# Kernel tuning notes

Hardware: AMD Instinct MI355X
Metric: run time of the kernel (lower is better)

## Reference

```python
import jax, jax.numpy as jnp
import numpy as np

B, V, D = 8, 1024, 512
H = 8
HD = D // H
MAX_HOP = 8


def setup_inputs() -> dict:
    key = jax.random.key(0)
    ks = jax.random.split(key, 5)
    x = jax.random.normal(ks[0], (B, V, D), dtype=jnp.float32)
    w_qkv = jax.random.normal(ks[1], (D, 3 * D), dtype=jnp.float32) * (D ** -0.5)
    w_out = jax.random.normal(ks[2], (D, D), dtype=jnp.float32) * (D ** -0.5)
    b_out = jnp.zeros((D,), dtype=jnp.float32)
    rpe_bias = jax.random.normal(ks[3], (H, MAX_HOP + 1), dtype=jnp.float32) * 0.02
    hop_matrix = jax.random.randint(ks[4], (V, V), 0, MAX_HOP + 1, dtype=jnp.int32)
    return {"x": x, "w_qkv": w_qkv, "w_out": w_out, "b_out": b_out,
            "rpe_bias": rpe_bias, "hop_matrix": hop_matrix}


def reference(x, w_qkv, w_out, b_out, rpe_bias, hop_matrix):
    b, v, d = x.shape
    scale = HD ** -0.5
    qkv = x @ w_qkv                                   # [B, V, 3D]
    q, k, val = jnp.split(qkv, 3, axis=-1)
    # [B, V, D] -> [B, H, V, HD]
    def split_heads(t):
        return t.reshape(b, v, H, HD).transpose(0, 2, 1, 3)
    q, k, val = split_heads(q), split_heads(k), split_heads(val)
    scores = jnp.einsum('bhvd,bhwd->bhvw', q, k)      # [B, H, V, V]
    bias = rpe_bias[:, hop_matrix]                    # gather -> [H, V, V]
    attn = jax.nn.softmax((scores + bias[None]) * scale, axis=-1)
    out_heads = jnp.einsum('bhvw,bhwd->bhvd', attn, val)
    out = out_heads.transpose(0, 2, 1, 3).reshape(b, v, d)
    out = out @ w_out + b_out
    return out, attn
```

## Files before the change

### kernel.cpp

```cpp
#include <hip/hip_runtime.h>

typedef __attribute__((ext_vector_type(8))) short bf16x8;
typedef __attribute__((ext_vector_type(4))) float f32x4;

#define MFMA16(A,B,C) __builtin_amdgcn_mfma_f32_16x16x32_bf16(A,B,C,0,0,0)

__device__ __forceinline__ unsigned short f2bf(float f){
  unsigned int u = __float_as_uint(f);
  u += 0x7FFFu + ((u >> 16) & 1u);
  return (unsigned short)(u >> 16);
}
__device__ __forceinline__ float bf2f(unsigned short s){
  return __uint_as_float(((unsigned int)s) << 16);
}
__device__ __forceinline__ int swz(int row, int kbyte){
  return (row * 128 + kbyte) ^ ((row & 7) << 4);
}

__global__ __launch_bounds__(256) void k_prep(
    const float* __restrict__ w_qkv, const float* __restrict__ w_out,
    unsigned short* __restrict__ wqT, unsigned short* __restrict__ woT)
{
  int idx = blockIdx.x * 256 + threadIdx.x;
  if (idx < 1536 * 512) {
    int n = idx >> 9, kq = idx & 511;
    wqT[idx] = f2bf(w_qkv[(size_t)kq * 1536 + n]);
  } else {
    int j = idx - 1536 * 512;
    int n = j >> 9, kq = j & 511;
    woT[j] = f2bf(w_out[(size_t)kq * 512 + n]);
  }
}

__global__ __launch_bounds__(256) void k_qkv(
    const float* __restrict__ x, const unsigned short* __restrict__ wqT,
    unsigned short* __restrict__ q, unsigned short* __restrict__ k_,
    unsigned short* __restrict__ valT)
{
  __shared__ char lds[32768];
  char* At = lds; char* Bt = lds + 16384;
  const int tid = threadIdx.x;
  const int wid = tid >> 6, lane = tid & 63, g = lane >> 4, r = lane & 15;
  const int wm = wid >> 1, wn = wid & 1;
  const int m0 = blockIdx.x * 128, n0 = blockIdx.y * 128;

  f32x4 acc[4][4];
#pragma unroll
  for (int a = 0; a < 4; ++a)
#pragma unroll
    for (int b = 0; b < 4; ++b) acc[a][b] = (f32x4){0.f, 0.f, 0.f, 0.f};

  for (int kt = 0; kt < 8; ++kt) {
    const int k0 = kt * 64;
    __syncthreads();
#pragma unroll
    for (int it = 0; it < 8; ++it) {
      int c = tid + it * 256;
      int row = c >> 4, c4 = c & 15;
      float4 xv = *reinterpret_cast<const float4*>(x + (size_t)(m0 + row) * 512 + k0 + c4 * 4);
      uint2 hv;
      hv.x = (unsigned)f2bf(xv.x) | ((unsigned)f2bf(xv.y) << 16);
      hv.y = (unsigned)f2bf(xv.z) | ((unsigned)f2bf(xv.w) << 16);
      *reinterpret_cast<uint2*>(At + swz(row, c4 * 8)) = hv;
    }
#pragma unroll
    for (int it = 0; it < 4; ++it) {
      int c = tid + it * 256;
      int row = c >> 3, c8 = c & 7;
      *reinterpret_cast<uint4*>(Bt + swz(row, c8 * 16)) =
          *reinterpret_cast<const uint4*>(wqT + (size_t)(n0 + row) * 512 + k0 + c8 * 8);
    }
    __syncthreads();
#pragma unroll
    for (int kk = 0; kk < 2; ++kk) {
      bf16x8 af[4], bf[4];
      const int kb = (kk * 32 + 8 * g) * 2;
#pragma unroll
      for (int mi = 0; mi < 4; ++mi)
        af[mi] = *reinterpret_cast<const bf16x8*>(At + swz(wm * 64 + mi * 16 + r, kb));
#pragma unroll
      for (int ni = 0; ni < 4; ++ni)
        bf[ni] = *reinterpret_cast<const bf16x8*>(Bt + swz(wn * 64 + ni * 16 + r, kb));
#pragma unroll
      for (int mi = 0; mi < 4; ++mi)
#pragma unroll
        for (int ni = 0; ni < 4; ++ni)
          acc[mi][ni] = MFMA16(af[mi], bf[ni], acc[mi][ni]);
    }
  }
  const int s = n0 >> 9;
#pragma unroll
  for (int mi = 0; mi < 4; ++mi)
#pragma unroll
    for (int ni = 0; ni < 4; ++ni)
#pragma unroll
      for (int i = 0; i < 4; ++i) {
        int m = m0 + wm * 64 + mi * 16 + 4 * g + i;
        int n = n0 + wn * 64 + ni * 16 + r;
        int b = m >> 10, v = m & 1023;
        int cc = n & 511, h = cc >> 6, d = cc & 63;
        int bh = b * 8 + h;
        unsigned short bfv = f2bf(acc[mi][ni][i]);
        if (s == 2)      valT[((size_t)bh * 64 + d) * 1024 + v] = bfv;
        else if (s == 0) q [((size_t)bh * 1024 + v) * 64 + d] = bfv;
        else             k_[((size_t)bh * 1024 + v) * 64 + d] = bfv;
      }
}

__global__ __launch_bounds__(256) void k_attn(
    const unsigned short* __restrict__ q, const unsigned short* __restrict__ k_,
    const unsigned short* __restrict__ valT,
    const float* __restrict__ rpe_bias, const int* __restrict__ hop,
    float* __restrict__ attn, unsigned short* __restrict__ oh)
{
  __shared__ float S[16 * 1028];
  __shared__ float rpe[9];
  const int tid = threadIdx.x;
  const int wid = tid >> 6, lane = tid & 63, g = lane >> 4, r = lane & 15;
  const int blk = blockIdx.x;
  const int vt = blk & 63, bh = blk >> 6, h = bh & 7;
  const int v0 = vt * 16;
  if (tid < 9) rpe[tid] = rpe_bias[h * 9 + tid];

  const unsigned short* qp = q + ((size_t)bh * 1024 + v0) * 64;
  bf16x8 qf[2];
#pragma unroll
  for (int kk = 0; kk < 2; ++kk)
    qf[kk] = *reinterpret_cast<const bf16x8*>(qp + r * 64 + kk * 32 + 8 * g);
  __syncthreads();

  const unsigned short* kb = k_ + (size_t)bh * 65536;
  for (int ct = 0; ct < 16; ++ct) {
    int cb = wid * 256 + ct * 16;
    f32x4 acc = (f32x4){0.f, 0.f, 0.f, 0.f};
#pragma unroll
    for (int kk = 0; kk < 2; ++kk) {
      bf16x8 kf = *reinterpret_cast<const bf16x8*>(kb + (size_t)(cb + r) * 64 + kk * 32 + 8 * g);
      acc = MFMA16(qf[kk], kf, acc);
    }
    int wcol = cb + r;
#pragma unroll
    for (int i = 0; i < 4; ++i) {
      int vl = 4 * g + i;
      int hv = hop[(size_t)(v0 + vl) * 1024 + wcol];
      S[vl * 1028 + wcol] = (acc[i] + rpe[hv]) * 0.125f;
    }
  }
  __syncthreads();

#pragma unroll
  for (int rr = 0; rr < 4; ++rr) {
    int row = wid * 4 + rr;
    float* Sr = S + row * 1028;
    float e[16];
    float m = -1e30f;
#pragma unroll
    for (int j = 0; j < 16; ++j) { e[j] = Sr[lane + 64 * j]; m = fmaxf(m, e[j]); }
#pragma unroll
    for (int o = 32; o; o >>= 1) m = fmaxf(m, __shfl_xor(m, o, 64));
    float sum = 0.f;
#pragma unroll
    for (int j = 0; j < 16; ++j) { e[j] = __expf(e[j] - m); sum += e[j]; }
#pragma unroll
    for (int o = 32; o; o >>= 1) sum += __shfl_xor(sum, o, 64);
    float inv = 1.0f / sum;
    float* ar = attn + ((size_t)bh * 1024 + v0 + row) * 1024;
#pragma unroll
    for (int j = 0; j < 16; ++j) {
      float a = e[j] * inv;
      int col = lane + 64 * j;
      Sr[col] = a;
      ar[col] = a;
    }
  }
  __syncthreads();

  const unsigned short* vT = valT + ((size_t)bh * 64 + wid * 16) * 1024;
  f32x4 acc = (f32x4){0.f, 0.f, 0.f, 0.f};
  for (int kc = 0; kc < 32; ++kc) {
    const float* ap = S + r * 1028 + kc * 32 + 8 * g;
    float4 p0 = *reinterpret_cast<const float4*>(ap);
    float4 p1 = *reinterpret_cast<const float4*>(ap + 4);
    bf16x8 af;
    af[0] = (short)f2bf(p0.x); af[1] = (short)f2bf(p0.y);
    af[2] = (short)f2bf(p0.z); af[3] = (short)f2bf(p0.w);
    af[4] = (short)f2bf(p1.x); af[5] = (short)f2bf(p1.y);
    af[6] = (short)f2bf(p1.z); af[7] = (short)f2bf(p1.w);
    bf16x8 bfr = *reinterpret_cast<const bf16x8*>(vT + (size_t)r * 1024 + kc * 32 + 8 * g);
    acc = MFMA16(af, bfr, acc);
  }
  const int b = bh >> 3;
#pragma unroll
  for (int i = 0; i < 4; ++i) {
    size_t oi = ((size_t)(b * 1024 + v0 + 4 * g + i)) * 512 + h * 64 + wid * 16 + r;
    oh[oi] = f2bf(acc[i]);
  }
}

__global__ __launch_bounds__(256) void k_out(
    const unsigned short* __restrict__ oh, const unsigned short* __restrict__ woT,
    const float* __restrict__ b_out, float* __restrict__ out)
{
  __shared__ char lds[32768];
  char* At = lds; char* Bt = lds + 16384;
  const int tid = threadIdx.x;
  const int wid = tid >> 6, lane = tid & 63, g = lane >> 4, r = lane & 15;
  const int wm = wid >> 1, wn = wid & 1;
  const int m0 = blockIdx.x * 128, n0 = blockIdx.y * 128;

  f32x4 acc[4][4];
#pragma unroll
  for (int a = 0; a < 4; ++a)
#pragma unroll
    for (int b = 0; b < 4; ++b) acc[a][b] = (f32x4){0.f, 0.f, 0.f, 0.f};

  for (int kt = 0; kt < 8; ++kt) {
    const int k0 = kt * 64;
    __syncthreads();
#pragma unroll
    for (int it = 0; it < 4; ++it) {
      int c = tid + it * 256;
      int row = c >> 3, c8 = c & 7;
      *reinterpret_cast<uint4*>(At + swz(row, c8 * 16)) =
          *reinterpret_cast<const uint4*>(oh + (size_t)(m0 + row) * 512 + k0 + c8 * 8);
      *reinterpret_cast<uint4*>(Bt + swz(row, c8 * 16)) =
          *reinterpret_cast<const uint4*>(woT + (size_t)(n0 + row) * 512 + k0 + c8 * 8);
    }
    __syncthreads();
#pragma unroll
    for (int kk = 0; kk < 2; ++kk) {
      bf16x8 a4[4], b4[4];
      const int kb = (kk * 32 + 8 * g) * 2;
#pragma unroll
      for (int mi = 0; mi < 4; ++mi)
        a4[mi] = *reinterpret_cast<const bf16x8*>(At + swz(wm * 64 + mi * 16 + r, kb));
#pragma unroll
      for (int ni = 0; ni < 4; ++ni)
        b4[ni] = *reinterpret_cast<const bf16x8*>(Bt + swz(wn * 64 + ni * 16 + r, kb));
#pragma unroll
      for (int mi = 0; mi < 4; ++mi)
#pragma unroll
        for (int ni = 0; ni < 4; ++ni)
          acc[mi][ni] = MFMA16(a4[mi], b4[ni], acc[mi][ni]);
    }
  }
#pragma unroll
  for (int mi = 0; mi < 4; ++mi)
#pragma unroll
    for (int ni = 0; ni < 4; ++ni)
#pragma unroll
      for (int i = 0; i < 4; ++i) {
        int m = m0 + wm * 64 + mi * 16 + 4 * g + i;
        int n = n0 + wn * 64 + ni * 16 + r;
        out[(size_t)m * 512 + n] = acc[mi][ni][i] + b_out[n];
      }
}

extern "C" void kernel_launch(void* const* d_in, const int* in_sizes, int n_in,
                              void* d_out, int out_size, void* d_ws, size_t ws_size,
                              hipStream_t stream) {
  const float *x = nullptr, *w_qkv = nullptr, *w_out = nullptr,
              *b_out = nullptr, *rpe = nullptr;
  const int* hop = nullptr;
  for (int i = 0; i < n_in; ++i) {
    switch (in_sizes[i]) {
      case 4194304: x     = (const float*)d_in[i]; break;
      case 786432:  w_qkv = (const float*)d_in[i]; break;
      case 262144:  w_out = (const float*)d_in[i]; break;
      case 512:     b_out = (const float*)d_in[i]; break;
      case 72:      rpe   = (const float*)d_in[i]; break;
      case 1048576: hop   = (const int*)d_in[i];   break;
    }
  }

  float* out  = (float*)d_out;
  float* attn = out + (size_t)4194304;

  char* ws = (char*)d_ws;
  unsigned short* q_   = (unsigned short*)(ws);
  unsigned short* k_   = (unsigned short*)(ws + (size_t) 8388608);
  unsigned short* valT = (unsigned short*)(ws + (size_t)16777216);
  unsigned short* oh   = (unsigned short*)(ws + (size_t)25165824);
  unsigned short* wqT  = (unsigned short*)(ws + (size_t)33554432);
  unsigned short* woT  = (unsigned short*)(ws + (size_t)35127296);

  k_prep<<<dim3(4096), dim3(256), 0, stream>>>(w_qkv, w_out, wqT, woT);
  k_qkv<<<dim3(64, 12), dim3(256), 0, stream>>>(x, wqT, q_, k_, valT);
  k_attn<<<dim3(4096), dim3(256), 0, stream>>>(q_, k_, valT, rpe, hop, attn, oh);
  k_out<<<dim3(64, 4), dim3(256), 0, stream>>>(oh, woT, b_out, out);
}
```

Before: 228.5 us.

## Keep attention scores in registers and precompute transposed bf16 RPE bias

Adds a k_bias kernel that gathers rpe_bias by hop_matrix once per head into a transposed bf16 table. This replaces the per-block int32 hop gathers, which were repeated for all 8 batches. The attention kernel now keeps scores in registers, does the softmax with cross-wave reductions through a small LDS buffer, and stores bf16 probabilities in LDS instead of a fp32 score matrix. This cuts LDS traffic and raises occupancy. It also switches the attn and out writes to nontemporal stores, at the cost of an extra 16MB bias buffer and bf16 rounding of the bias.

```diff
diff --git a/kernel.cpp b/kernel.cpp
--- a/kernel.cpp
+++ b/kernel.cpp
@@ -29,6 +29,33 @@
     int j = idx - 1536 * 512;
     int n = j >> 9, kq = j & 511;
     woT[j] = f2bf(w_out[(size_t)kq * 512 + n]);
+  }
+}
+
+__global__ __launch_bounds__(256) void k_bias(
+    const int* __restrict__ hop, const float* __restrict__ rpe_bias,
+    unsigned short* __restrict__ biasT)
+{
+  __shared__ int ht[64][65];
+  __shared__ float rl[72];
+  const int tid = threadIdx.x;
+  if (tid < 72) rl[tid] = rpe_bias[tid];
+  const int wt = blockIdx.x & 15, vt = blockIdx.x >> 4;
+  const int c = tid & 63, r4 = tid >> 6;
+#pragma unroll
+  for (int it = 0; it < 16; ++it) {
+    int r = r4 * 16 + it;
+    ht[r][c] = hop[(size_t)(vt * 64 + r) * 1024 + wt * 64 + c];
+  }
+  __syncthreads();
+#pragma unroll
+  for (int it = 0; it < 16; ++it) {
+    int wr = r4 * 16 + it;
+    int hv = ht[c][wr];
+#pragma unroll
+    for (int h = 0; h < 8; ++h)
+      biasT[((size_t)h << 20) + (size_t)(wt * 64 + wr) * 1024 + vt * 64 + c] =
+          f2bf(rl[h * 9 + hv]);
   }
 }
 
@@ -107,70 +134,101 @@
       }
 }
 
-__global__ __launch_bounds__(256) void k_attn(
+__global__ __launch_bounds__(256, 3) void k_attn(
     const unsigned short* __restrict__ q, const unsigned short* __restrict__ k_,
     const unsigned short* __restrict__ valT,
-    const float* __restrict__ rpe_bias, const int* __restrict__ hop,
+    const unsigned short* __restrict__ biasT,
     float* __restrict__ attn, unsigned short* __restrict__ oh)
 {
-  __shared__ float S[16 * 1028];
-  __shared__ float rpe[9];
+  __shared__ unsigned short P[16 * 1040];
+  __shared__ float red[2][4][16];
   const int tid = threadIdx.x;
   const int wid = tid >> 6, lane = tid & 63, g = lane >> 4, r = lane & 15;
   const int blk = blockIdx.x;
   const int vt = blk & 63, bh = blk >> 6, h = bh & 7;
   const int v0 = vt * 16;
-  if (tid < 9) rpe[tid] = rpe_bias[h * 9 + tid];
 
   const unsigned short* qp = q + ((size_t)bh * 1024 + v0) * 64;
   bf16x8 qf[2];
 #pragma unroll
   for (int kk = 0; kk < 2; ++kk)
     qf[kk] = *reinterpret_cast<const bf16x8*>(qp + r * 64 + kk * 32 + 8 * g);
+
+  const unsigned short* kb = k_ + (size_t)bh * 65536;
+  const unsigned short* bb = biasT + ((size_t)h << 20);
+  f32x4 s[16];
+#pragma unroll
+  for (int ct = 0; ct < 16; ++ct) {
+    const int wcol = wid * 256 + ct * 16 + r;
+    ushort4 bv = *reinterpret_cast<const ushort4*>(bb + (size_t)wcol * 1024 + v0 + 4 * g);
+    f32x4 acc = (f32x4){0.f, 0.f, 0.f, 0.f};
+#pragma unroll
+    for (int kk = 0; kk < 2; ++kk) {
+      bf16x8 kf = *reinterpret_cast<const bf16x8*>(kb + (size_t)wcol * 64 + kk * 32 + 8 * g);
+      acc = MFMA16(qf[kk], kf, acc);
+    }
+    s[ct][0] = (acc[0] + bf2f(bv.x)) * 0.125f;
+    s[ct][1] = (acc[1] + bf2f(bv.y)) * 0.125f;
+    s[ct][2] = (acc[2] + bf2f(bv.z)) * 0.125f;
+    s[ct][3] = (acc[3] + bf2f(bv.w)) * 0.125f;
+  }
+
+  float mx[4] = {-1e30f, -1e30f, -1e30f, -1e30f};
+#pragma unroll
+  for (int ct = 0; ct < 16; ++ct)
+#pragma unroll
+    for (int i = 0; i < 4; ++i) mx[i] = fmaxf(mx[i], s[ct][i]);
+#pragma unroll
+  for (int o = 1; o <= 8; o <<= 1)
+#pragma unroll
+    for (int i = 0; i < 4; ++i) mx[i] = fmaxf(mx[i], __shfl_xor(mx[i], o, 64));
+  if (r == 0)
+#pragma unroll
+    for (int i = 0; i < 4; ++i) red[0][wid][4 * g + i] = mx[i];
   __syncthreads();
-
-  const unsigned short* kb = k_ + (size_t)bh * 65536;
+#pragma unroll
+  for (int i = 0; i < 4; ++i) {
+    float M = red[0][0][4 * g + i];
+#pragma unroll
+    for (int w = 1; w < 4; ++w) M = fmaxf(M, red[0][w][4 * g + i]);
+    mx[i] = M;
+  }
+
+  float sm[4] = {0.f, 0.f, 0.f, 0.f};
+#pragma unroll
+  for (int ct = 0; ct < 16; ++ct)
+#pragma unroll
+    for (int i = 0; i < 4; ++i) {
+      float e = __expf(s[ct][i] - mx[i]);
+      s[ct][i] = e;
+      sm[i] += e;
+    }
+#pragma unroll
+  for (int o = 1; o <= 8; o <<= 1)
+#pragma unroll
+    for (int i = 0; i < 4; ++i) sm[i] += __shfl_xor(sm[i], o, 64);
+  if (r == 0)
+#pragma unroll
+    for (int i = 0; i < 4; ++i) red[1][wid][4 * g + i] = sm[i];
+  __syncthreads();
+  float inv[4];
+#pragma unroll
+  for (int i = 0; i < 4; ++i) {
+    float T = red[1][0][4 * g + i] + red[1][1][4 * g + i] +
+              red[1][2][4 * g + i] + red[1][3][4 * g + i];
+    inv[i] = 1.0f / T;
+  }
+
+  float* ab = attn + ((size_t)bh * 1024 + v0) * 1024;
+#pragma unroll
   for (int ct = 0; ct < 16; ++ct) {
-    int cb = wid * 256 + ct * 16;
-    f32x4 acc = (f32x4){0.f, 0.f, 0.f, 0.f};
-#pragma unroll
-    for (int kk = 0; kk < 2; ++kk) {
-      bf16x8 kf = *reinterpret_cast<const bf16x8*>(kb + (size_t)(cb + r) * 64 + kk * 32 + 8 * g);
-      acc = MFMA16(qf[kk], kf, acc);
-    }
-    int wcol = cb + r;
+    const int col = wid * 256 + ct * 16 + r;
 #pragma unroll
     for (int i = 0; i < 4; ++i) {
-      int vl = 4 * g + i;
-      int hv = hop[(size_t)(v0 + vl) * 1024 + wcol];
-      S[vl * 1028 + wcol] = (acc[i] + rpe[hv]) * 0.125f;
-    }
-  }
-  __syncthreads();
-
-#pragma unroll
-  for (int rr = 0; rr < 4; ++rr) {
-    int row = wid * 4 + rr;
-    float* Sr = S + row * 1028;
-    float e[16];
-    float m = -1e30f;
-#pragma unroll
-    for (int j = 0; j < 16; ++j) { e[j] = Sr[lane + 64 * j]; m = fmaxf(m, e[j]); }
-#pragma unroll
-    for (int o = 32; o; o >>= 1) m = fmaxf(m, __shfl_xor(m, o, 64));
-    float sum = 0.f;
-#pragma unroll
-    for (int j = 0; j < 16; ++j) { e[j] = __expf(e[j] - m); sum += e[j]; }
-#pragma unroll
-    for (int o = 32; o; o >>= 1) sum += __shfl_xor(sum, o, 64);
-    float inv = 1.0f / sum;
-    float* ar = attn + ((size_t)bh * 1024 + v0 + row) * 1024;
-#pragma unroll
-    for (int j = 0; j < 16; ++j) {
-      float a = e[j] * inv;
-      int col = lane + 64 * j;
-      Sr[col] = a;
-      ar[col] = a;
+      const int row = 4 * g + i;
+      float a = s[ct][i] * inv[i];
+      __builtin_nontemporal_store(a, ab + (size_t)row * 1024 + col);
+      P[row * 1040 + col] = f2bf(a);
     }
   }
   __syncthreads();
@@ -178,16 +236,9 @@
   const unsigned short* vT = valT + ((size_t)bh * 64 + wid * 16) * 1024;
   f32x4 acc = (f32x4){0.f, 0.f, 0.f, 0.f};
   for (int kc = 0; kc < 32; ++kc) {
-    const float* ap = S + r * 1028 + kc * 32 + 8 * g;
-    float4 p0 = *reinterpret_cast<const float4*>(ap);
-    float4 p1 = *reinterpret_cast<const float4*>(ap + 4);
-    bf16x8 af;
-    af[0] = (short)f2bf(p0.x); af[1] = (short)f2bf(p0.y);
-    af[2] = (short)f2bf(p0.z); af[3] = (short)f2bf(p0.w);
-    af[4] = (short)f2bf(p1.x); af[5] = (short)f2bf(p1.y);
-    af[6] = (short)f2bf(p1.z); af[7] = (short)f2bf(p1.w);
-    bf16x8 bfr = *reinterpret_cast<const bf16x8*>(vT + (size_t)r * 1024 + kc * 32 + 8 * g);
-    acc = MFMA16(af, bfr, acc);
+    bf16x8 pa = *reinterpret_cast<const bf16x8*>(&P[r * 1040 + kc * 32 + 8 * g]);
+    bf16x8 vb = *reinterpret_cast<const bf16x8*>(vT + (size_t)r * 1024 + kc * 32 + 8 * g);
+    acc = MFMA16(pa, vb, acc);
   }
   const int b = bh >> 3;
 #pragma unroll
@@ -252,7 +303,7 @@
       for (int i = 0; i < 4; ++i) {
         int m = m0 + wm * 64 + mi * 16 + 4 * g + i;
         int n = n0 + wn * 64 + ni * 16 + r;
-        out[(size_t)m * 512 + n] = acc[mi][ni][i] + b_out[n];
+        __builtin_nontemporal_store(acc[mi][ni][i] + b_out[n], out + (size_t)m * 512 + n);
       }
 }
 
@@ -277,15 +328,17 @@
   float* attn = out + (size_t)4194304;
 
   char* ws = (char*)d_ws;
-  unsigned short* q_   = (unsigned short*)(ws);
-  unsigned short* k_   = (unsigned short*)(ws + (size_t) 8388608);
-  unsigned short* valT = (unsigned short*)(ws + (size_t)16777216);
-  unsigned short* oh   = (unsigned short*)(ws + (size_t)25165824);
-  unsigned short* wqT  = (unsigned short*)(ws + (size_t)33554432);
-  unsigned short* woT  = (unsigned short*)(ws + (size_t)35127296);
+  unsigned short* q_    = (unsigned short*)(ws);
+  unsigned short* k_    = (unsigned short*)(ws + (size_t) 8388608);
+  unsigned short* valT  = (unsigned short*)(ws + (size_t)16777216);
+  unsigned short* oh    = (unsigned short*)(ws + (size_t)25165824);
+  unsigned short* wqT   = (unsigned short*)(ws + (size_t)33554432);
+  unsigned short* woT   = (unsigned short*)(ws + (size_t)35127296);
+  unsigned short* biasT = (unsigned short*)(ws + (size_t)35651584);
 
   k_prep<<<dim3(4096), dim3(256), 0, stream>>>(w_qkv, w_out, wqT, woT);
+  k_bias<<<dim3(256), dim3(256), 0, stream>>>(hop, rpe, biasT);
   k_qkv<<<dim3(64, 12), dim3(256), 0, stream>>>(x, wqT, q_, k_, valT);
-  k_attn<<<dim3(4096), dim3(256), 0, stream>>>(q_, k_, valT, rpe, hop, attn, oh);
+  k_attn<<<dim3(4096), dim3(256), 0, stream>>>(q_, k_, valT, biasT, attn, oh);
   k_out<<<dim3(64, 4), dim3(256), 0, stream>>>(oh, woT, b_out, out);
 }
```

New measurement: 247.0 us. 1.08x slower.
